# Kernel tuning notes

Measured on AMD Instinct MI355X. Metric: run time of the kernel, lower is better.

Reference implementation:

```python
import jax, jax.numpy as jnp
import numpy as np

U1, U2, FEAT = 24, 48, 16
LN_EPS = 1e-3  # tf.keras LayerNormalization default


def _ln(x, gamma, beta):
    mu = jnp.mean(x, axis=-1, keepdims=True)
    var = jnp.mean(jnp.square(x - mu), axis=-1, keepdims=True)
    return (x - mu) * jax.lax.rsqrt(var + LN_EPS) * gamma + beta


def setup_inputs() -> dict:
    key = jax.random.key(0)
    ks = jax.random.split(key, 8)
    B, T = 8192, 256
    sequence = jax.random.normal(ks[0], (B, T, FEAT), dtype=jnp.float32)
    s = 0.1
    return {
        "sequence": sequence,
        "W1": jax.random.normal(ks[1], (FEAT, U1), dtype=jnp.float32) * s,
        "b1": jnp.zeros((U1,), jnp.float32),
        "Wr1": jax.random.normal(ks[2], (U1, U1), dtype=jnp.float32) * s,
        "br1": jnp.zeros((U1,), jnp.float32),
        "g1": jnp.ones((U1,), jnp.float32),
        "be1": jnp.zeros((U1,), jnp.float32),
        "W2": jax.random.normal(ks[3], (U1, U2), dtype=jnp.float32) * s,
        "b2": jnp.zeros((U2,), jnp.float32),
        "Wr2": jax.random.normal(ks[4], (U2, U2), dtype=jnp.float32) * s,
        "br2": jnp.zeros((U2,), jnp.float32),
        "g2": jnp.ones((U2,), jnp.float32),
        "be2": jnp.zeros((U2,), jnp.float32),
        "Wout": jax.random.normal(ks[5], (U2, 1), dtype=jnp.float32) * s,
        "bout": jnp.zeros((1,), jnp.float32),
    }


def reference(sequence, W1, b1, Wr1, br1, g1, be1, W2, b2, Wr2, br2, g2, be2, Wout, bout):
    B = sequence.shape[0]
    xs = jnp.swapaxes(sequence, 0, 1)  # [T, B, F]

    def step(carry, inp):
        s1, s2 = carry
        x = inp @ W1 + b1 + s1
        ns1 = jnp.tanh(x @ Wr1 + br1)
        h = _ln(ns1, g1, be1)
        y = h @ W2 + b2 + s2
        ns2 = jnp.tanh(y @ Wr2 + br2)
        return (ns1, ns2), None

    init = (jnp.zeros((B, U1), sequence.dtype), jnp.zeros((B, U2), sequence.dtype))
    (s1, s2), _ = jax.lax.scan(step, init, xs)
    last_out = _ln(s2, g2, be2)  # output of final timestep (return_sequences=False)
    return jax.nn.sigmoid(last_out @ Wout + bout)  # [B, 1]
```

## Files before the change

### kernel.cpp

```cpp
#include <hip/hip_runtime.h>

#define T_STEPS 256
#define FEAT 16
#define U1 24
#define U2 48
#define ROWB 144
#define SLOTS 8

typedef short bf16x8 __attribute__((ext_vector_type(8)));
typedef float f32x4 __attribute__((ext_vector_type(4)));

__device__ __forceinline__ unsigned short f2bf(float f) {
    unsigned u = __float_as_uint(f);
    u += 0x7fffu + ((u >> 16) & 1u);
    return (unsigned short)(u >> 16);
}

#if defined(__has_builtin)
#if __has_builtin(__builtin_amdgcn_cvt_pk_bf16_f32)
#define HAVE_PKBF16 1
#endif
#endif

__device__ __forceinline__ unsigned pk2(float a, float b) {
#ifdef HAVE_PKBF16
    typedef __bf16 bf2 __attribute__((ext_vector_type(2)));
    union { bf2 v; unsigned u; } cv;
    cv.v = __builtin_amdgcn_cvt_pk_bf16_f32(a, b);
    return cv.u;
#else
    return (unsigned)f2bf(a) | ((unsigned)f2bf(b) << 16);
#endif
}
__device__ __forceinline__ float bfr(float x) {
    return __uint_as_float(((unsigned)f2bf(x)) << 16);
}
__device__ __forceinline__ float fast_tanh(float z) {
    return 1.0f - 2.0f / (1.0f + __expf(2.0f * z));
}

union FragU { bf16x8 v; unsigned u[4]; };

#define MFMA(A, B, C) __builtin_amdgcn_mfma_f32_16x16x32_bf16((A), (B), (C), 0, 0, 0)

__device__ __forceinline__ void bar_sync() {
    asm volatile("" ::: "memory");
    __builtin_amdgcn_s_waitcnt(0xC07F);
    __builtin_amdgcn_s_barrier();
    asm volatile("" ::: "memory");
}

__global__ __launch_bounds__(128) void rnn_kernel(
    const float* __restrict__ seq,
    const float* __restrict__ W1, const float* __restrict__ b1,
    const float* __restrict__ Wr1, const float* __restrict__ br1,
    const float* __restrict__ g1, const float* __restrict__ be1,
    const float* __restrict__ W2, const float* __restrict__ b2,
    const float* __restrict__ Wr2, const float* __restrict__ br2,
    const float* __restrict__ g2, const float* __restrict__ be2,
    const float* __restrict__ Wout, const float* __restrict__ bout,
    float* __restrict__ out)
{
    __shared__ __align__(16) unsigned char tr0[16 * ROWB];
    __shared__ __align__(16) unsigned char tr1[16 * ROWB];
    __shared__ __align__(16) unsigned char ring[SLOTS * 16 * ROWB];

    const int tid = threadIdx.x;
    const int w = tid >> 6;
    const int lane = tid & 63;
    const int j15 = lane & 15;
    const int g = lane >> 4;
    const f32x4 z4 = {0.f, 0.f, 0.f, 0.f};

    if (w == 0) {
        bf16x8 A1[2], A2[2];
#pragma unroll
        for (int t = 0; t < 2; ++t) {
            const int m = 16 * t + j15;
            FragU f1, f2;
#pragma unroll
            for (int j = 0; j < 8; ++j) {
                const int k = 8 * g + j;
                float v1 = 0.f, v2 = 0.f;
                if (m < U1) {
                    if (k < FEAT) v1 = W1[k * U1 + m];
                    else if (k == FEAT) v1 = b1[m];
                    if (k < U1) v2 = Wr1[k * U1 + m];
                    else if (k == U1) v2 = br1[m];
                } else if (m == U1 && k == FEAT) {
                    v1 = 1.f;
                }
                f1.v[j] = (short)f2bf(v1);
                f2.v[j] = (short)f2bf(v2);
            }
            A1[t] = f1.v; A2[t] = f2.v;
        }
        const unsigned cdw0 = (g == 2) ? 0x00003F80u : 0u;
        unsigned char* const xrow = tr0 + j15 * ROWB;

        const float* sp = seq + (size_t)(blockIdx.x * 16 + j15) * (T_STEPS * FEAT) + 8 * g;
        const bool ld = (lane < 32);

        f32x4 s1[2] = {z4, z4};

        auto pstep = [&](int t, const float4 ca, const float4 cb) {
            FragU inf;
            const unsigned p0 = pk2(ca.x, ca.y), p1 = pk2(ca.z, ca.w);
            const unsigned p2 = pk2(cb.x, cb.y), p3 = pk2(cb.z, cb.w);
            const bool lo = (g < 2);
            inf.u[0] = lo ? p0 : cdw0;
            inf.u[1] = lo ? p1 : 0u;
            inf.u[2] = lo ? p2 : 0u;
            inf.u[3] = lo ? p3 : 0u;

            const f32x4 x0 = MFMA(A1[0], inf.v, s1[0]);
            const f32x4 x1 = MFMA(A1[1], inf.v, s1[1]);

            *(uint2*)(xrow + 8 * g)      = make_uint2(pk2(x0[0], x0[1]), pk2(x0[2], x0[3]));
            *(uint2*)(xrow + 32 + 8 * g) = make_uint2(pk2(x1[0], x1[1]), pk2(x1[2], x1[3]));
            const bf16x8 xf = *(const bf16x8*)(xrow + 16 * g);

            const f32x4 d0 = MFMA(A2[0], xf, z4);
            const f32x4 d1 = MFMA(A2[1], xf, z4);
            float n1a[4], n1b[4], qa[4], qb[4];
#pragma unroll
            for (int r = 0; r < 4; ++r) {
                n1a[r] = fast_tanh(d0[r]); n1b[r] = fast_tanh(d1[r]);
                qa[r] = n1a[r] * n1a[r];   qb[r] = n1b[r] * n1b[r];
                s1[0][r] = n1a[r];         s1[1][r] = n1b[r];
            }
            unsigned char* rp = ring + ((size_t)(t & (SLOTS - 1)) * 16 + j15) * ROWB;
            *(uint2*)(rp + 8 * g)      = make_uint2(pk2(n1a[0], n1a[1]), pk2(n1a[2], n1a[3]));
            *(uint2*)(rp + 32 + 8 * g) = make_uint2(pk2(n1b[0], n1b[1]), pk2(n1b[2], n1b[3]));
            *(uint2*)(rp + 64 + 8 * g) = make_uint2(pk2(qa[0], qa[1]), pk2(qa[2], qa[3]));
            *(uint2*)(rp + 96 + 8 * g) = make_uint2(pk2(qb[0], qb[1]), pk2(qb[2], qb[3]));
        };

        float4 ca[4], cb[4], na[4], nb[4];
        if (ld) {
#pragma unroll
            for (int i = 0; i < 4; ++i) {
                ca[i] = *(const float4*)(sp + i * 16);
                cb[i] = *(const float4*)(sp + i * 16 + 4);
            }
        }
#pragma unroll 1
        for (int j = 0; j < 64; ++j) {
            const int jn = (j + 1 < 64) ? j + 1 : j;
            if (ld) {
#pragma unroll
                for (int i = 0; i < 4; ++i) {
                    na[i] = *(const float4*)(sp + (4 * jn + i) * 16);
                    nb[i] = *(const float4*)(sp + (4 * jn + i) * 16 + 4);
                }
            }
#pragma unroll
            for (int i = 0; i < 4; ++i) pstep(4 * j + i, ca[i], cb[i]);
            bar_sync();
#pragma unroll
            for (int i = 0; i < 4; ++i) { ca[i] = na[i]; cb[i] = nb[i]; }
        }
        bar_sync();
    } else {
        for (int i = lane; i < 16 * ROWB / 4; i += 64) ((unsigned*)tr1)[i] = 0u;
        if (lane < 16) *(unsigned short*)(tr1 + lane * ROWB + 96) = 0x3F80;

        bf16x8 A3a[4], A3b3, A4[3][2];
#pragma unroll
        for (int t = 0; t < 3; ++t) {
            const int m = 16 * t + j15;
            FragU f3, f4a, f4b;
#pragma unroll
            for (int j = 0; j < 8; ++j) {
                const int k = 8 * g + j;
                const float v3 = (k < U1) ? g1[k] * W2[k * U2 + m] : 0.f;
                const int kb = 32 + k;
                const float va = Wr2[k * U2 + m];
                const float vb = (kb < U2) ? Wr2[kb * U2 + m] : (kb == U2 ? br2[m] : 0.f);
                f3.v[j] = (short)f2bf(v3);
                f4a.v[j] = (short)f2bf(va);
                f4b.v[j] = (short)f2bf(vb);
            }
            A3a[t] = f3.v; A4[t][0] = f4a.v; A4[t][1] = f4b.v;
        }
        {
            FragU fa, fb;
#pragma unroll
            for (int j = 0; j < 8; ++j) {
                const int k = 8 * g + j;
                fa.v[j] = ((j15 & 3) == 0 && k < U1) ? (short)0x3F80 : (short)0;
                fb.v[j] = ((j15 & 3) == 1 && k < U1) ? (short)0x3F80 : (short)0;
            }
            A3a[3] = fa.v; A3b3 = fb.v;
        }
        float cC[12], dC[12];
#pragma unroll
        for (int i = 0; i < 12; ++i) {
            const int m = 16 * (i >> 2) + 4 * g + (i & 3);
            float cc = 0.f, dd = b2[m];
            for (int k = 0; k < U1; ++k) {
                const float wq = bfr(g1[k] * W2[k * U2 + m]);
                cc += wq;
                dd += be1[k] * W2[k * U2 + m];
            }
            cC[i] = cc; dC[i] = dd;
        }
        unsigned char* const yrow = tr1 + j15 * ROWB;
        f32x4 s2[3] = {z4, z4, z4};

        auto cstep = [&](int t) {
            const unsigned char* rp = ring + ((size_t)(t & (SLOTS - 1)) * 16 + j15) * ROWB;
            const bf16x8 hf0 = *(const bf16x8*)(rp + 16 * g);
            const bf16x8 hf1 = *(const bf16x8*)(rp + 64 + 16 * g);

            f32x4 sAcc = MFMA(A3a[3], hf0, z4);
            sAcc = MFMA(A3b3, hf1, sAcc);
            const f32x4 P0 = MFMA(A3a[0], hf0, z4);
            const f32x4 P1 = MFMA(A3a[1], hf0, z4);
            const f32x4 P2 = MFMA(A3a[2], hf0, z4);

            const float mu = sAcc[0] * (1.f / U1);
            const float var = sAcc[1] * (1.f / U1) - mu * mu;
            const float rs = rsqrtf(var + 1e-3f);

            float y[12];
#pragma unroll
            for (int r = 0; r < 4; ++r) {
                y[r]     = fmaf(rs, fmaf(-mu, cC[r],     P0[r]), dC[r]     + s2[0][r]);
                y[4 + r] = fmaf(rs, fmaf(-mu, cC[4 + r], P1[r]), dC[4 + r] + s2[1][r]);
                y[8 + r] = fmaf(rs, fmaf(-mu, cC[8 + r], P2[r]), dC[8 + r] + s2[2][r]);
            }

            *(uint2*)(yrow + 8 * g)      = make_uint2(pk2(y[0], y[1]), pk2(y[2], y[3]));
            *(uint2*)(yrow + 32 + 8 * g) = make_uint2(pk2(y[4], y[5]), pk2(y[6], y[7]));
            *(uint2*)(yrow + 64 + 8 * g) = make_uint2(pk2(y[8], y[9]), pk2(y[10], y[11]));
            const bf16x8 yf0 = *(const bf16x8*)(yrow + 16 * g);
            const bf16x8 yf1 = *(const bf16x8*)(yrow + 64 + 16 * g);

#pragma unroll
            for (int t3 = 0; t3 < 3; ++t3) {
                f32x4 e = MFMA(A4[t3][0], yf0, z4);
                e = MFMA(A4[t3][1], yf1, e);
#pragma unroll
                for (int r = 0; r < 4; ++r) s2[t3][r] = fast_tanh(e[r]);
            }
        };

        bar_sync();
#pragma unroll 1
        for (int j = 0; j < 64; ++j) {
#pragma unroll
            for (int i = 0; i < 4; ++i) cstep(4 * j + i);
            bar_sync();
        }

        float g2r[12], be2r[12], wor[12];
#pragma unroll
        for (int r = 0; r < 12; ++r) {
            const int n = 16 * (r >> 2) + 4 * g + (r & 3);
            g2r[r] = g2[n]; be2r[r] = be2[n]; wor[r] = Wout[n];
        }
        float sm = 0.f, sq = 0.f;
#pragma unroll
        for (int tt = 0; tt < 3; ++tt)
#pragma unroll
            for (int r = 0; r < 4; ++r) { const float v = s2[tt][r]; sm += v; sq += v * v; }
        sm += __shfl_xor(sm, 16, 64); sq += __shfl_xor(sq, 16, 64);
        sm += __shfl_xor(sm, 32, 64); sq += __shfl_xor(sq, 32, 64);
        const float mu = sm * (1.f / U2);
        const float var = sq * (1.f / U2) - mu * mu;
        const float rs = rsqrtf(var + 1e-3f);
        float p = 0.f;
#pragma unroll
        for (int tt = 0; tt < 3; ++tt)
#pragma unroll
            for (int r = 0; r < 4; ++r)
                p += ((s2[tt][r] - mu) * rs * g2r[4 * tt + r] + be2r[4 * tt + r]) * wor[4 * tt + r];
        p += __shfl_xor(p, 16, 64);
        p += __shfl_xor(p, 32, 64);
        if (lane < 16) {
            const float z = p + bout[0];
            out[blockIdx.x * 16 + lane] = 1.0f / (1.0f + __expf(-z));
        }
    }
}

extern "C" void kernel_launch(void* const* d_in, const int* in_sizes, int n_in,
                              void* d_out, int out_size, void* d_ws, size_t ws_size,
                              hipStream_t stream) {
    const float* seq  = (const float*)d_in[0];
    const float* W1   = (const float*)d_in[1];
    const float* b1   = (const float*)d_in[2];
    const float* Wr1  = (const float*)d_in[3];
    const float* br1  = (const float*)d_in[4];
    const float* g1   = (const float*)d_in[5];
    const float* be1  = (const float*)d_in[6];
    const float* W2   = (const float*)d_in[7];
    const float* b2   = (const float*)d_in[8];
    const float* Wr2  = (const float*)d_in[9];
    const float* br2  = (const float*)d_in[10];
    const float* g2   = (const float*)d_in[11];
    const float* be2  = (const float*)d_in[12];
    const float* Wout = (const float*)d_in[13];
    const float* bout = (const float*)d_in[14];
    float* out = (float*)d_out;

    const int B = in_sizes[0] / (T_STEPS * FEAT);
    const int grid = B / 16;
    rnn_kernel<<<grid, 128, 0, stream>>>(seq, W1, b1, Wr1, br1, g1, be1,
                                         W2, b2, Wr2, br2, g2, be2, Wout, bout, out);
}
```

Baseline: 352.6 us.

## Double ring slots, halve barriers, use fast exp2/rcp/rsq intrinsics

Grows the producer/consumer LDS ring from 8 to 16 slots and processes 8 timesteps per barrier instead of 4, halving the number of block-wide barriers. Input prefetch becomes two register buffers loaded in a ping-pong pattern. tanh, rsqrt and sigmoid now call hardware exp2/rcp/rsq intrinsics, and the fallback bf16 packing uses a perm instruction. The y-row stores are reordered so the first fragment load is issued earlier. This costs more LDS, some added padding per slot, more live registers, and slightly lower-precision transcendentals.

```diff
diff --git a/kernel.cpp b/kernel.cpp
--- a/kernel.cpp
+++ b/kernel.cpp
@@ -4,8 +4,10 @@
 #define FEAT 16
 #define U1 24
 #define U2 48
+#define SLOTS 16
 #define ROWB 144
-#define SLOTS 8
+#define SLOT_B (16 * ROWB + 128)
+#define SUMS_OFF (16 * ROWB)
 
 typedef short bf16x8 __attribute__((ext_vector_type(8)));
 typedef float f32x4 __attribute__((ext_vector_type(4)));
@@ -29,14 +31,40 @@
     cv.v = __builtin_amdgcn_cvt_pk_bf16_f32(a, b);
     return cv.u;
 #else
-    return (unsigned)f2bf(a) | ((unsigned)f2bf(b) << 16);
+    unsigned ua = __float_as_uint(a), ub = __float_as_uint(b);
+    ua += 0x7fffu + ((ua >> 16) & 1u);
+    ub += 0x7fffu + ((ub >> 16) & 1u);
+    return __builtin_amdgcn_perm(ub, ua, 0x07060302);
 #endif
 }
 __device__ __forceinline__ float bfr(float x) {
     return __uint_as_float(((unsigned)f2bf(x)) << 16);
 }
+
+__device__ __forceinline__ float rcp_fast(float x) {
+#if __has_builtin(__builtin_amdgcn_rcpf)
+    return __builtin_amdgcn_rcpf(x);
+#else
+    return 1.0f / x;
+#endif
+}
+__device__ __forceinline__ float exp2_fast(float x) {
+#if __has_builtin(__builtin_amdgcn_exp2f)
+    return __builtin_amdgcn_exp2f(x);
+#else
+    return exp2f(x);
+#endif
+}
+__device__ __forceinline__ float rsq_fast(float x) {
+#if __has_builtin(__builtin_amdgcn_rsqf)
+    return __builtin_amdgcn_rsqf(x);
+#else
+    return rsqrtf(x);
+#endif
+}
 __device__ __forceinline__ float fast_tanh(float z) {
-    return 1.0f - 2.0f / (1.0f + __expf(2.0f * z));
+    const float e = exp2_fast(2.885390081777927f * z);
+    return fmaf(-2.0f, rcp_fast(1.0f + e), 1.0f);
 }
 
 union FragU { bf16x8 v; unsigned u[4]; };
@@ -61,9 +89,9 @@
     const float* __restrict__ Wout, const float* __restrict__ bout,
     float* __restrict__ out)
 {
+    __shared__ __align__(16) unsigned char ring[SLOTS * SLOT_B];
     __shared__ __align__(16) unsigned char tr0[16 * ROWB];
     __shared__ __align__(16) unsigned char tr1[16 * ROWB];
-    __shared__ __align__(16) unsigned char ring[SLOTS * 16 * ROWB];
 
     const int tid = threadIdx.x;
     const int w = tid >> 6;
@@ -96,7 +124,7 @@
             A1[t] = f1.v; A2[t] = f2.v;
         }
         const unsigned cdw0 = (g == 2) ? 0x00003F80u : 0u;
-        unsigned char* const xrow = tr0 + j15 * ROWB;
+        const bool lo = (g < 2);
 
         const float* sp = seq + (size_t)(blockIdx.x * 16 + j15) * (T_STEPS * FEAT) + 8 * g;
         const bool ld = (lane < 32);
@@ -107,7 +135,6 @@
             FragU inf;
             const unsigned p0 = pk2(ca.x, ca.y), p1 = pk2(ca.z, ca.w);
             const unsigned p2 = pk2(cb.x, cb.y), p3 = pk2(cb.z, cb.w);
-            const bool lo = (g < 2);
             inf.u[0] = lo ? p0 : cdw0;
             inf.u[1] = lo ? p1 : 0u;
             inf.u[2] = lo ? p2 : 0u;
@@ -116,6 +143,7 @@
             const f32x4 x0 = MFMA(A1[0], inf.v, s1[0]);
             const f32x4 x1 = MFMA(A1[1], inf.v, s1[1]);
 
+            unsigned char* xrow = tr0 + (size_t)j15 * ROWB;
             *(uint2*)(xrow + 8 * g)      = make_uint2(pk2(x0[0], x0[1]), pk2(x0[2], x0[3]));
             *(uint2*)(xrow + 32 + 8 * g) = make_uint2(pk2(x1[0], x1[1]), pk2(x1[2], x1[3]));
             const bf16x8 xf = *(const bf16x8*)(xrow + 16 * g);
@@ -129,36 +157,36 @@
                 qa[r] = n1a[r] * n1a[r];   qb[r] = n1b[r] * n1b[r];
                 s1[0][r] = n1a[r];         s1[1][r] = n1b[r];
             }
-            unsigned char* rp = ring + ((size_t)(t & (SLOTS - 1)) * 16 + j15) * ROWB;
+            unsigned char* rp = ring + (size_t)(t & (SLOTS - 1)) * SLOT_B + (size_t)j15 * ROWB;
             *(uint2*)(rp + 8 * g)      = make_uint2(pk2(n1a[0], n1a[1]), pk2(n1a[2], n1a[3]));
             *(uint2*)(rp + 32 + 8 * g) = make_uint2(pk2(n1b[0], n1b[1]), pk2(n1b[2], n1b[3]));
             *(uint2*)(rp + 64 + 8 * g) = make_uint2(pk2(qa[0], qa[1]), pk2(qa[2], qa[3]));
             *(uint2*)(rp + 96 + 8 * g) = make_uint2(pk2(qb[0], qb[1]), pk2(qb[2], qb[3]));
         };
 
-        float4 ca[4], cb[4], na[4], nb[4];
-        if (ld) {
-#pragma unroll
-            for (int i = 0; i < 4; ++i) {
-                ca[i] = *(const float4*)(sp + i * 16);
-                cb[i] = *(const float4*)(sp + i * 16 + 4);
-            }
-        }
+        float4 ca[4], cb4[4], na[4], nb[4];
+        auto load4 = [&](float4* A, float4* Bv, int grp) {
+            if (ld) {
+                const float* q = sp + (size_t)grp * 64;
+#pragma unroll
+                for (int i = 0; i < 4; ++i) {
+                    A[i] = *(const float4*)(q + 16 * i);
+                    Bv[i] = *(const float4*)(q + 16 * i + 4);
+                }
+            }
+        };
+        load4(ca, cb4, 0);
+        load4(na, nb, 1);
+
 #pragma unroll 1
-        for (int j = 0; j < 64; ++j) {
-            const int jn = (j + 1 < 64) ? j + 1 : j;
-            if (ld) {
-#pragma unroll
-                for (int i = 0; i < 4; ++i) {
-                    na[i] = *(const float4*)(sp + (4 * jn + i) * 16);
-                    nb[i] = *(const float4*)(sp + (4 * jn + i) * 16 + 4);
-                }
-            }
-#pragma unroll
-            for (int i = 0; i < 4; ++i) pstep(4 * j + i, ca[i], cb[i]);
+        for (int j = 0; j < 32; ++j) {
+#pragma unroll
+            for (int i = 0; i < 4; ++i) pstep(8 * j + i, ca[i], cb4[i]);
+            load4(ca, cb4, (2 * j + 2 < 64) ? 2 * j + 2 : 63);
+#pragma unroll
+            for (int i = 0; i < 4; ++i) pstep(8 * j + 4 + i, na[i], nb[i]);
+            load4(na, nb, (2 * j + 3 < 64) ? 2 * j + 3 : 63);
             bar_sync();
-#pragma unroll
-            for (int i = 0; i < 4; ++i) { ca[i] = na[i]; cb[i] = nb[i]; }
         }
         bar_sync();
     } else {
@@ -199,19 +227,18 @@
             const int m = 16 * (i >> 2) + 4 * g + (i & 3);
             float cc = 0.f, dd = b2[m];
             for (int k = 0; k < U1; ++k) {
-                const float wq = bfr(g1[k] * W2[k * U2 + m]);
-                cc += wq;
+                cc += bfr(g1[k] * W2[k * U2 + m]);
                 dd += be1[k] * W2[k * U2 + m];
             }
             cC[i] = cc; dC[i] = dd;
         }
-        unsigned char* const yrow = tr1 + j15 * ROWB;
+        unsigned char* const yrow = tr1 + (size_t)j15 * ROWB;
         f32x4 s2[3] = {z4, z4, z4};
 
         auto cstep = [&](int t) {
-            const unsigned char* rp = ring + ((size_t)(t & (SLOTS - 1)) * 16 + j15) * ROWB;
-            const bf16x8 hf0 = *(const bf16x8*)(rp + 16 * g);
-            const bf16x8 hf1 = *(const bf16x8*)(rp + 64 + 16 * g);
+            const unsigned char* sb = ring + (size_t)(t & (SLOTS - 1)) * SLOT_B;
+            const bf16x8 hf0 = *(const bf16x8*)(sb + (size_t)j15 * ROWB + 16 * g);
+            const bf16x8 hf1 = *(const bf16x8*)(sb + (size_t)j15 * ROWB + 64 + 16 * g);
 
             f32x4 sAcc = MFMA(A3a[3], hf0, z4);
             sAcc = MFMA(A3b3, hf1, sAcc);
@@ -221,20 +248,21 @@
 
             const float mu = sAcc[0] * (1.f / U1);
             const float var = sAcc[1] * (1.f / U1) - mu * mu;
-            const float rs = rsqrtf(var + 1e-3f);
+            const float rs = rsq_fast(var + 1e-3f);
 
             float y[12];
 #pragma unroll
             for (int r = 0; r < 4; ++r) {
                 y[r]     = fmaf(rs, fmaf(-mu, cC[r],     P0[r]), dC[r]     + s2[0][r]);
                 y[4 + r] = fmaf(rs, fmaf(-mu, cC[4 + r], P1[r]), dC[4 + r] + s2[1][r]);
-                y[8 + r] = fmaf(rs, fmaf(-mu, cC[8 + r], P2[r]), dC[8 + r] + s2[2][r]);
-            }
-
+            }
             *(uint2*)(yrow + 8 * g)      = make_uint2(pk2(y[0], y[1]), pk2(y[2], y[3]));
             *(uint2*)(yrow + 32 + 8 * g) = make_uint2(pk2(y[4], y[5]), pk2(y[6], y[7]));
+            const bf16x8 yf0 = *(const bf16x8*)(yrow + 16 * g);
+#pragma unroll
+            for (int r = 0; r < 4; ++r)
+                y[8 + r] = fmaf(rs, fmaf(-mu, cC[8 + r], P2[r]), dC[8 + r] + s2[2][r]);
             *(uint2*)(yrow + 64 + 8 * g) = make_uint2(pk2(y[8], y[9]), pk2(y[10], y[11]));
-            const bf16x8 yf0 = *(const bf16x8*)(yrow + 16 * g);
             const bf16x8 yf1 = *(const bf16x8*)(yrow + 64 + 16 * g);
 
 #pragma unroll
@@ -248,9 +276,9 @@
 
         bar_sync();
 #pragma unroll 1
-        for (int j = 0; j < 64; ++j) {
-#pragma unroll
-            for (int i = 0; i < 4; ++i) cstep(4 * j + i);
+        for (int j = 0; j < 32; ++j) {
+#pragma unroll
+            for (int i = 0; i < 8; ++i) cstep(8 * j + i);
             bar_sync();
         }
 
@@ -269,7 +297,7 @@
         sm += __shfl_xor(sm, 32, 64); sq += __shfl_xor(sq, 32, 64);
         const float mu = sm * (1.f / U2);
         const float var = sq * (1.f / U2) - mu * mu;
-        const float rs = rsqrtf(var + 1e-3f);
+        const float rs = rsq_fast(var + 1e-3f);
         float p = 0.f;
 #pragma unroll
         for (int tt = 0; tt < 3; ++tt)
@@ -280,7 +308,7 @@
         p += __shfl_xor(p, 32, 64);
         if (lane < 16) {
             const float z = p + bout[0];
-            out[blockIdx.x * 16 + lane] = 1.0f / (1.0f + __expf(-z));
+            out[blockIdx.x * 16 + lane] = rcp_fast(1.0f + exp2_fast(-1.4426950408889634f * z));
         }
     }
 }
```

After: 371.2 us. 1.05x slower.
